# Kernel tuning notes

Measured on AMD Instinct MI355X. Metric: run time of the kernel, lower is better.

## Reference

```python
import jax, jax.numpy as jnp
import numpy as np

N_PAPER, N_AUTHOR = 200000, 100000
D_PAPER, D_AUTHOR = 128, 64
H, OUT = 64, 32
E_CITES, E_WRITES = 4000000, 2000000


def _gcn(x, W, b, src, dst, n):
    # GCNConv with default add_self_loops=True, symmetric normalization
    xl = x @ W
    deg = jnp.zeros((n,), xl.dtype).at[dst].add(1.0) + 1.0  # +1 for self loop
    dis = jax.lax.rsqrt(deg)
    norm = dis[src] * dis[dst]
    out = jax.ops.segment_sum(xl[src] * norm[:, None], dst, num_segments=n)
    out = out + xl * (dis * dis)[:, None]  # self-loop term: norm_ii = 1/deg_i
    return out + b


def _sage(x_src, x_dst, Wl, bl, Wr, src, dst, n_dst):
    # SAGEConv: mean neighbor aggregation -> lin_l, plus root lin_r on dst
    ones = jnp.ones(src.shape, x_src.dtype)
    cnt = jnp.maximum(jax.ops.segment_sum(ones, dst, num_segments=n_dst), 1.0)
    mean = jax.ops.segment_sum(x_src[src], dst, num_segments=n_dst) / cnt[:, None]
    return mean @ Wl + bl + x_dst @ Wr


def _gat(x_src, x_dst, Ws, Wd, a_s, a_d, b, src, dst, n_dst):
    # GATConv heads=1, bipartite, add_self_loops=False, leaky_relu slope 0.2
    xs = x_src @ Ws  # [Ns, H]
    xd = x_dst @ Wd  # [Nd, H]
    a_src = xs @ a_s  # [Ns]
    a_dst = xd @ a_d  # [Nd]
    e = a_src[src] + a_dst[dst]
    e = jnp.where(e > 0, e, 0.2 * e)
    m = jax.ops.segment_max(e, dst, num_segments=n_dst)
    m = jnp.where(jnp.isfinite(m), m, 0.0)  # nodes with no in-edges
    ex = jnp.exp(e - m[dst])
    denom = jax.ops.segment_sum(ex, dst, num_segments=n_dst)
    alpha = ex / denom[dst]
    out = jax.ops.segment_sum(alpha[:, None] * xs[src], dst, num_segments=n_dst)
    return out + b


def _forward(x_paper, x_author, params, cites_src, cites_dst, writes_src, writes_dst):
    for (gW, gb, sWl, sbl, sWr, aWs, aWd, aas, aad, ab) in params:
        p_gcn = _gcn(x_paper, gW, gb, cites_src, cites_dst, N_PAPER)
        p_sage = _sage(x_author, x_paper, sWl, sbl, sWr, writes_src, writes_dst, N_PAPER)
        # rev_writes: paper -> author, i.e. src=writes_dst (paper), dst=writes_src (author)
        a_gat = _gat(x_paper, x_author, aWs, aWd, aas, aad, ab, writes_dst, writes_src, N_AUTHOR)
        x_paper = jax.nn.relu(p_gcn + p_sage)  # HeteroConv aggr='sum'
        x_author = jax.nn.relu(a_gat)
    return x_paper, x_author


def setup_inputs() -> dict:
    key = jax.random.key(0)
    ks = jax.random.split(key, 40)
    rn = lambda i, shp, s=0.1: jax.random.normal(ks[i], shp, jnp.float32) * s
    inp = {}
    inp['x_paper'] = rn(0, (N_PAPER, D_PAPER), 1.0)
    inp['x_author'] = rn(1, (N_AUTHOR, D_AUTHOR), 1.0)
    dims = [(D_PAPER, D_AUTHOR), (H, H)]
    i = 2
    for l, (dp, da) in enumerate(dims):
        inp[f'gcn_W{l}'] = rn(i, (dp, H)); i += 1
        inp[f'gcn_b{l}'] = jnp.zeros((H,), jnp.float32)
        inp[f'sage_Wl{l}'] = rn(i, (da, H)); i += 1
        inp[f'sage_bl{l}'] = jnp.zeros((H,), jnp.float32)
        inp[f'sage_Wr{l}'] = rn(i, (dp, H)); i += 1
        inp[f'gat_Ws{l}'] = rn(i, (dp, H)); i += 1
        inp[f'gat_Wd{l}'] = rn(i, (da, H)); i += 1
        inp[f'gat_as{l}'] = rn(i, (H,)); i += 1
        inp[f'gat_ad{l}'] = rn(i, (H,)); i += 1
        inp[f'gat_b{l}'] = jnp.zeros((H,), jnp.float32)
    inp['lin_W'] = rn(i, (H, OUT)); i += 1
    inp['lin_b'] = jnp.zeros((OUT,), jnp.float32)
    inp['cites_src'] = jax.random.randint(ks[30], (E_CITES,), 0, N_PAPER)
    inp['cites_dst'] = jax.random.randint(ks[31], (E_CITES,), 0, N_PAPER)
    inp['writes_src'] = jax.random.randint(ks[32], (E_WRITES,), 0, N_AUTHOR)
    inp['writes_dst'] = jax.random.randint(ks[33], (E_WRITES,), 0, N_PAPER)
    return inp


def reference(x_paper, x_author,
              gcn_W0, gcn_b0, sage_Wl0, sage_bl0, sage_Wr0,
              gat_Ws0, gat_Wd0, gat_as0, gat_ad0, gat_b0,
              gcn_W1, gcn_b1, sage_Wl1, sage_bl1, sage_Wr1,
              gat_Ws1, gat_Wd1, gat_as1, gat_ad1, gat_b1,
              lin_W, lin_b,
              cites_src, cites_dst, writes_src, writes_dst):
    params = [
        (gcn_W0, gcn_b0, sage_Wl0, sage_bl0, sage_Wr0, gat_Ws0, gat_Wd0, gat_as0, gat_ad0, gat_b0),
        (gcn_W1, gcn_b1, sage_Wl1, sage_bl1, sage_Wr1, gat_Ws1, gat_Wd1, gat_as1, gat_ad1, gat_b1),
    ]
    _, x_author_out = _forward(x_paper, x_author, params, cites_src, cites_dst, writes_src, writes_dst)
    return x_author_out @ lin_W + lin_b
```

## Files before the change

kernel.cpp:

```cpp
#include <hip/hip_runtime.h>
#include <hip/hip_bf16.h>

#define NP 200000
#define NA 100000
#define DP 128
#define HD 64
#define EC 4000000
#define EW 2000000
#define NSCAN (2 * NP + NA)
#define NBUCK 4
#define CAPC 64
#define CAPW 48
#define CAPA 64

typedef __hip_bfloat16 bf16;
typedef __attribute__((ext_vector_type(8))) short short8;
typedef __attribute__((ext_vector_type(4))) float f32x4;

__device__ __forceinline__ float bf2f(bf16 h) { return __bfloat162float(h); }

__device__ __forceinline__ short8 pack8(float4 a, float4 b) {
    union {
        short8 s;
        unsigned u[4];
    } r;
    __hip_bfloat162 h;
    h = __float22bfloat162_rn(float2{a.x, a.y});
    r.u[0] = *reinterpret_cast<unsigned*>(&h);
    h = __float22bfloat162_rn(float2{a.z, a.w});
    r.u[1] = *reinterpret_cast<unsigned*>(&h);
    h = __float22bfloat162_rn(float2{b.x, b.y});
    r.u[2] = *reinterpret_cast<unsigned*>(&h);
    h = __float22bfloat162_rn(float2{b.z, b.w});
    r.u[3] = *reinterpret_cast<unsigned*>(&h);
    return r.s;
}


__global__ __launch_bounds__(256) void fill_pass_kernel(const int* __restrict__ cs,
                                                        const int* __restrict__ cd,
                                                        const int* __restrict__ ws,
                                                        const int* __restrict__ wd,
                                                        int* __restrict__ CUR,
                                                        int* __restrict__ colC,
                                                        int* __restrict__ colWd,
                                                        int* __restrict__ colWa, int bucket) {
    long i = (long)blockIdx.x * 256 + threadIdx.x;
    if (i < EC) {
        int d = __builtin_nontemporal_load(&cd[i]);
        if ((int)(((long)d * NBUCK) / NP) != bucket) return;
        int s = __builtin_nontemporal_load(&cs[i]);
        int pos = atomicAdd(&CUR[d * 4], 1);
        if (pos < CAPC) colC[(size_t)d * CAPC + pos] = s;
    } else if (i < (long)EC + EW) {
        long e = i - EC;
        int d = __builtin_nontemporal_load(&wd[e]);
        int a = __builtin_nontemporal_load(&ws[e]);
        if ((int)(((long)d * NBUCK) / NP) == bucket) {
            int pos = atomicAdd(&CUR[(NP + d) * 4], 1);
            if (pos < CAPW) colWd[(size_t)d * CAPW + pos] = a;
        }
        if ((int)(((long)a * NBUCK) / NA) == bucket) {
            int pos = atomicAdd(&CUR[(2 * NP + a) * 4], 1);
            if (pos < CAPA) colWa[(size_t)a * CAPA + pos] = d;
        }
    }
}


__global__ __launch_bounds__(256) void conv_author_kernel(const float* __restrict__ XA,
                                                          const float* __restrict__ wvec,
                                                          bf16* __restrict__ XAbf,
                                                          float* __restrict__ adst) {
    __shared__ float vs[64];
    if (threadIdx.x < 64) vs[threadIdx.x] = wvec[threadIdx.x];
    __syncthreads();
    int r = blockIdx.x * 4 + (threadIdx.x >> 6);
    int lane = threadIdx.x & 63;
    float x = XA[(size_t)r * 64 + lane];
    XAbf[(size_t)r * 64 + lane] = __float2bfloat16(x);
    float p = x * vs[lane];
#pragma unroll
    for (int o = 32; o > 0; o >>= 1) p += __shfl_xor(p, o, 64);
    if (lane == 0) adst[r] = p;
}


__global__ void wprep_kernel(const float* __restrict__ Wg, const float* __restrict__ Wl,
                             const float* __restrict__ Wr, const float* __restrict__ Ws0,
                             const float* __restrict__ Ws1, short* __restrict__ WF,
                             const float* __restrict__ Wd0, const float* __restrict__ ad0,
                             const float* __restrict__ Wd1, const float* __restrict__ ad1,
                             float* __restrict__ wvec0, float* __restrict__ wvec1) {
    int bid = blockIdx.x;
    int lane = threadIdx.x;
    if (bid >= 64) {
        const float* Wd = (bid == 64) ? Wd0 : Wd1;
        const float* ad = (bid == 64) ? ad0 : ad1;
        float* wv = (bid == 64) ? wvec0 : wvec1;
        float s = 0.f;
        for (int c = 0; c < 64; c++) s += Wd[lane * 64 + c] * ad[c];
        wv[lane] = s;
        return;
    }
    int q = lane & 15, g = lane >> 4;
    int m, r;
    size_t dst;
    if (bid < 16) {
        m = 0; r = bid; dst = 0;
    } else if (bid < 40) {
        m = 1; r = bid - 16; dst = 8192;
    } else if (bid < 56) {
        m = 2; r = bid - 40; dst = 20480;
    } else {
        m = 3; r = bid - 56; dst = 28672;
    }
    int ks = r >> 2, n = r & 3;
    int col = n * 16 + q;
    float v[8];
#pragma unroll
    for (int j = 0; j < 8; j++) {
        int kr = ks * 32 + g * 8 + j;
        float x;
        if (m == 0) x = Wg[(size_t)kr * 64 + col];
        else if (m == 1) x = (kr < 64) ? Wl[(size_t)kr * 64 + col] : Wr[(size_t)(kr - 64) * 64 + col];
        else if (m == 2) x = Ws0[(size_t)kr * 64 + col];
        else x = Ws1[(size_t)kr * 64 + col];
        v[j] = x;
    }
    short8 s = pack8(float4{v[0], v[1], v[2], v[3]}, float4{v[4], v[5], v[6], v[7]});
    *reinterpret_cast<short8*>(WF + dst + ((size_t)r * 64 + lane) * 8) = s;
}


template <int K, int ASTRIDE, bool ABF16, bool ADOT, bool SCALE>
__global__ __launch_bounds__(256) void mfma_gemm_kernel(const void* __restrict__ Xv,
                                                        const short* __restrict__ Wf,
                                                        bf16* __restrict__ outb,
                                                        const float* __restrict__ avec,
                                                        float* __restrict__ adot,
                                                        const int* __restrict__ CURs) {
    int tid = threadIdx.x;
    int lane = tid & 63, q = lane & 15, g = lane >> 4;
    int rw = blockIdx.x * 64 + (tid >> 6) * 16;
    int arow = rw + q;
    f32x4 acc[4];
#pragma unroll
    for (int n = 0; n < 4; n++) acc[n] = f32x4{0.f, 0.f, 0.f, 0.f};
#pragma unroll
    for (int ks = 0; ks < K / 32; ks++) {
        short8 af;
        if constexpr (ABF16) {
            af = *reinterpret_cast<const short8*>((const bf16*)Xv + (size_t)arow * ASTRIDE +
                                                  ks * 32 + g * 8);
        } else {
            const float* xr = (const float*)Xv + (size_t)arow * ASTRIDE + ks * 32 + g * 8;
            float4 a0 = *reinterpret_cast<const float4*>(xr);
            float4 a1 = *reinterpret_cast<const float4*>(xr + 4);
            af = pack8(a0, a1);
        }
#pragma unroll
        for (int n = 0; n < 4; n++) {
            short8 bfr =
                *reinterpret_cast<const short8*>(Wf + ((size_t)(ks * 4 + n) * 64 + lane) * 8);
            acc[n] = __builtin_amdgcn_mfma_f32_16x16x32_bf16(af, bfr, acc[n], 0, 0, 0);
        }
    }
    float av[4];
    if constexpr (ADOT) {
#pragma unroll
        for (int n = 0; n < 4; n++) av[n] = avec[n * 16 + q];
    }
#pragma unroll
    for (int j = 0; j < 4; j++) {
        int R = rw + g * 4 + j;
        float sc = 1.f;
        if constexpr (SCALE) sc = rsqrtf((float)CURs[(unsigned)R * 4] + 1.0f);
#pragma unroll
        for (int n = 0; n < 4; n++) {
            outb[(size_t)R * 64 + n * 16 + q] = __float2bfloat16(acc[n][j] * sc);
        }
        if constexpr (ADOT) {
            float t = acc[0][j] * av[0] + acc[1][j] * av[1] + acc[2][j] * av[2] + acc[3][j] * av[3];
            t += __shfl_xor(t, 1, 64);
            t += __shfl_xor(t, 2, 64);
            t += __shfl_xor(t, 4, 64);
            t += __shfl_xor(t, 8, 64);
            if (q == 0) adot[R] = t;
        }
    }
}


__global__ __launch_bounds__(256) void mfma_sage_kernel(const bf16* B3s,
                                                        const float* __restrict__ XP,
                                                        const float* __restrict__ B2,
                                                        const float* __restrict__ bl,
                                                        const short* __restrict__ Wf, bf16* P1) {
    int tid = threadIdx.x;
    int lane = tid & 63, q = lane & 15, g = lane >> 4;
    int rw = blockIdx.x * 64 + (tid >> 6) * 16;
    int arow = rw + q;
    f32x4 acc[4];
#pragma unroll
    for (int n = 0; n < 4; n++) acc[n] = f32x4{0.f, 0.f, 0.f, 0.f};
#pragma unroll
    for (int ks = 0; ks < 6; ks++) {
        short8 af;
        if (ks < 2) {
            af = *reinterpret_cast<const short8*>(B3s + (size_t)arow * 128 + 64 + ks * 32 + g * 8);
        } else {
            const float* xr = XP + (size_t)arow * DP + (ks - 2) * 32 + g * 8;
            float4 a0 = *reinterpret_cast<const float4*>(xr);
            float4 a1 = *reinterpret_cast<const float4*>(xr + 4);
            af = pack8(a0, a1);
        }
#pragma unroll
        for (int n = 0; n < 4; n++) {
            short8 bfr =
                *reinterpret_cast<const short8*>(Wf + ((size_t)(ks * 4 + n) * 64 + lane) * 8);
            acc[n] = __builtin_amdgcn_mfma_f32_16x16x32_bf16(af, bfr, acc[n], 0, 0, 0);
        }
    }
    float blv[4];
#pragma unroll
    for (int n = 0; n < 4; n++) blv[n] = bl[n * 16 + q];
#pragma unroll
    for (int j = 0; j < 4; j++) {
        int R = rw + g * 4 + j;
#pragma unroll
        for (int n = 0; n < 4; n++) {
            int col = n * 16 + q;
            float v = acc[n][j] + B2[(size_t)R * 64 + col] + blv[n];
            P1[(size_t)R * 128 + col] = __float2bfloat16(fmaxf(v, 0.f));
        }
    }
}


__global__ __launch_bounds__(256) void paper_gather_kernel(const bf16* __restrict__ B1,
                                                           const bf16* __restrict__ XA,
                                                           const int* __restrict__ CUR,
                                                           const int* colC,
                                                           const int* __restrict__ colWd,
                                                           const float* __restrict__ gb,
                                                           float* __restrict__ B2, bf16* B3s) {
    int node = __builtin_amdgcn_readfirstlane(blockIdx.x * 4 + (threadIdx.x >> 6));
    unsigned lane = threadIdx.x & 63;
    int degc_t = CUR[(unsigned)node * 4];
    float dd = rsqrtf((float)degc_t + 1.0f);
    int degc = min(degc_t, CAPC);
    unsigned cb = (unsigned)node * CAPC;
    float acc = bf2f(B1[((unsigned)node << 6) + lane]);
    int e = 0;
    for (; e + 8 <= degc; e += 8) {
        unsigned off[8];
#pragma unroll
        for (int j = 0; j < 8; j++) off[j] = ((unsigned)colC[cb + e + j] << 6) + lane;
        float v[8];
#pragma unroll
        for (int j = 0; j < 8; j++) v[j] = bf2f(B1[off[j]]);
#pragma unroll
        for (int j = 0; j < 8; j++) acc += v[j];
    }
    for (; e + 4 <= degc; e += 4) {
        unsigned o0 = ((unsigned)colC[cb + e] << 6) + lane;
        unsigned o1 = ((unsigned)colC[cb + e + 1] << 6) + lane;
        unsigned o2 = ((unsigned)colC[cb + e + 2] << 6) + lane;
        unsigned o3 = ((unsigned)colC[cb + e + 3] << 6) + lane;
        float v0 = bf2f(B1[o0]), v1 = bf2f(B1[o1]);
        float v2 = bf2f(B1[o2]), v3 = bf2f(B1[o3]);
        acc += v0 + v1;
        acc += v2 + v3;
    }
    for (; e < degc; e++) acc += bf2f(B1[((unsigned)colC[cb + e] << 6) + lane]);
    B2[((unsigned)node << 6) + lane] = acc * dd + gb[lane];
    int degw_t = CUR[((unsigned)NP + node) * 4];
    float ic = 1.0f / fmaxf((float)degw_t, 1.0f);
    int degw = min(degw_t, CAPW);
    unsigned wb = (unsigned)node * CAPW;
    float s = 0.f;
    e = 0;
    for (; e + 8 <= degw; e += 8) {
        unsigned off[8];
#pragma unroll
        for (int j = 0; j < 8; j++) off[j] = ((unsigned)colWd[wb + e + j] << 6) + lane;
        float v[8];
#pragma unroll
        for (int j = 0; j < 8; j++) v[j] = bf2f(XA[off[j]]);
#pragma unroll
        for (int j = 0; j < 8; j++) s += v[j];
    }
    for (; e + 4 <= degw; e += 4) {
        unsigned o0 = ((unsigned)colWd[wb + e] << 6) + lane;
        unsigned o1 = ((unsigned)colWd[wb + e + 1] << 6) + lane;
        unsigned o2 = ((unsigned)colWd[wb + e + 2] << 6) + lane;
        unsigned o3 = ((unsigned)colWd[wb + e + 3] << 6) + lane;
        float v0 = bf2f(XA[o0]), v1 = bf2f(XA[o1]);
        float v2 = bf2f(XA[o2]), v3 = bf2f(XA[o3]);
        s += v0 + v1;
        s += v2 + v3;
    }
    for (; e < degw; e++) s += bf2f(XA[((unsigned)colWd[wb + e] << 6) + lane]);
    B3s[(unsigned)node * 128u + 64u + lane] = __float2bfloat16(s * ic);
}


__device__ __forceinline__ float lrelu(float v) { return v > 0.f ? v : 0.2f * v; }

__device__ __forceinline__ float rl_f(float v, int l) {
    return __int_as_float(__builtin_amdgcn_readlane(__float_as_int(v), l));
}

__device__ __forceinline__ void gat_phase(const bf16* __restrict__ XS, int pi, float xi, int deg,
                                          unsigned lane, float& accO, float& denO) {
    float den = xi;
#pragma unroll
    for (int o = 32; o > 0; o >>= 1) den += __shfl_xor(den, o, 64);
    float acc = 0.f;
    int l = 0;
    for (; l + 8 <= deg; l += 8) {
        float v[8];
#pragma unroll
        for (int j = 0; j < 8; j++) {
            unsigned pl = (unsigned)__builtin_amdgcn_readlane(pi, l + j);
            v[j] = bf2f(XS[(pl << 6) + lane]);
        }
#pragma unroll
        for (int j = 0; j < 8; j++) acc += rl_f(xi, l + j) * v[j];
    }
    for (; l < deg; l++) {
        unsigned pl = (unsigned)__builtin_amdgcn_readlane(pi, l);
        acc += rl_f(xi, l) * bf2f(XS[(pl << 6) + lane]);
    }
    accO = acc;
    denO = den;
}

__global__ __launch_bounds__(256) void gat_fused_kernel(
    const bf16* __restrict__ XS0, const bf16* __restrict__ XS1, const int* __restrict__ CUR,
    const int* __restrict__ colA, const float* __restrict__ asrc0,
    const float* __restrict__ asrc1, const float* __restrict__ adst0,
    const float* __restrict__ ab0, const float* __restrict__ wvec1,
    const float* __restrict__ ab1, const float* __restrict__ linW,
    const float* __restrict__ linb, float* __restrict__ out) {
    __shared__ float Ws[64 * 32];
    __shared__ float vbuf[4][64];
    __shared__ float lbs[32];
    int tid = threadIdx.x;
    for (int i = tid; i < 64 * 32; i += 256) Ws[i] = linW[i];
    if (tid < 32) lbs[tid] = linb[tid];
    __syncthreads();
    int wid = tid >> 6;
    int a = __builtin_amdgcn_readfirstlane(blockIdx.x * 4 + wid);
    unsigned lane = tid & 63;
    int deg = min(CUR[(2u * NP + a) * 4], CAPA);
    unsigned cb = (unsigned)a * CAPA;
    int pi = (lane < (unsigned)deg) ? colA[cb + lane] : 0;
    bool act = lane < (unsigned)deg;
    float x0 = act ? __expf(lrelu(asrc0[(unsigned)pi] + adst0[(unsigned)a])) : 0.f;
    float acc0, den0;
    gat_phase(XS0, pi, x0, deg, lane, acc0, den0);
    float inv0 = den0 > 0.f ? 1.f / den0 : 0.f;
    float val0 = fmaxf(acc0 * inv0 + ab0[lane], 0.f);
    float ada1 = val0 * wvec1[lane];
#pragma unroll
    for (int o = 32; o > 0; o >>= 1) ada1 += __shfl_xor(ada1, o, 64);
    float x1 = act ? __expf(lrelu(asrc1[(unsigned)pi] + ada1)) : 0.f;
    float acc1, den1;
    gat_phase(XS1, pi, x1, deg, lane, acc1, den1);
    float inv1 = den1 > 0.f ? 1.f / den1 : 0.f;
    vbuf[wid][lane] = fmaxf(acc1 * inv1 + ab1[lane], 0.f);
    __syncthreads();
    if (tid < 128) {
        int w = tid >> 5, c = tid & 31;
        int node = blockIdx.x * 4 + w;
        float s = lbs[c];
#pragma unroll
        for (int k = 0; k < 64; k++) s += vbuf[w][k] * Ws[k * 32 + c];
        out[(size_t)node * 32 + c] = s;
    }
}


static inline int cdivi(long a, long b) { return (int)((a + b - 1) / b); }

extern "C" void kernel_launch(void* const* d_in, const int* in_sizes, int n_in, void* d_out,
                              int out_size, void* d_ws, size_t ws_size, hipStream_t stream) {
    const float* x_paper = (const float*)d_in[0];
    const float* x_author = (const float*)d_in[1];
    const float* gcn_W0 = (const float*)d_in[2];
    const float* gcn_b0 = (const float*)d_in[3];
    const float* sage_Wl0 = (const float*)d_in[4];
    const float* sage_bl0 = (const float*)d_in[5];
    const float* sage_Wr0 = (const float*)d_in[6];
    const float* gat_Ws0 = (const float*)d_in[7];
    const float* gat_Wd0 = (const float*)d_in[8];
    const float* gat_as0 = (const float*)d_in[9];
    const float* gat_ad0 = (const float*)d_in[10];
    const float* gat_b0 = (const float*)d_in[11];
    const float* gat_Ws1 = (const float*)d_in[17];
    const float* gat_Wd1 = (const float*)d_in[18];
    const float* gat_as1 = (const float*)d_in[19];
    const float* gat_ad1 = (const float*)d_in[20];
    const float* gat_b1 = (const float*)d_in[21];
    const float* lin_W = (const float*)d_in[22];
    const float* lin_b = (const float*)d_in[23];
    const int* cites_src = (const int*)d_in[24];
    const int* cites_dst = (const int*)d_in[25];
    const int* writes_src = (const int*)d_in[26];
    const int* writes_dst = (const int*)d_in[27];

    float* out = (float*)d_out;

    char* base = (char*)d_ws;
    bf16* BF = (bf16*)base;
    base += (size_t)NP * 64 * 2;
    float* B2 = (float*)base;
    base += (size_t)NP * 64 * 4;
    int* colC = (int*)base;
    bf16* R3 = (bf16*)base;
    base += (size_t)NP * CAPC * 4;
    int* colWd = (int*)base;
    bf16* XS1 = (bf16*)base;
    base += (size_t)NP * CAPW * 4;
    int* colWa = (int*)base;
    base += (size_t)NA * CAPA * 4;
    bf16* XAbf = (bf16*)base;
    base += (size_t)NA * 64 * 2;
    int* CUR = (int*)base;
    base += (size_t)NSCAN * 4 * 4;
    float* asrc0 = (float*)base;
    float* asrc1 = asrc0 + NP;
    float* adst0 = asrc1 + NP;
    float* wvec0 = adst0 + NA;
    float* wvec1 = wvec0 + 64;
    short* WF = (short*)(wvec1 + 64);

    dim3 blk(256);
    const long EMERGED = (long)EC + EW;

    hipMemsetAsync(CUR, 0, (size_t)NSCAN * 4 * 4, stream);
    wprep_kernel<<<66, 64, 0, stream>>>(gcn_W0, sage_Wl0, sage_Wr0, gat_Ws0, gat_Ws1, WF, gat_Wd0,
                                        gat_ad0, gat_Wd1, gat_ad1, wvec0, wvec1);

    for (int b = 0; b < NBUCK; b++) {
        fill_pass_kernel<<<cdivi(EMERGED, 256), blk, 0, stream>>>(cites_src, cites_dst,
                                                                  writes_src, writes_dst, CUR,
                                                                  colC, colWd, colWa, b);
    }

    conv_author_kernel<<<NA / 4, blk, 0, stream>>>(x_author, wvec0, XAbf, adst0);

    mfma_gemm_kernel<DP, DP, false, false, true><<<NP / 64, blk, 0, stream>>>(x_paper, WF, BF,
                                                                              nullptr, nullptr,
                                                                              CUR);
    paper_gather_kernel<<<NP / 4, blk, 0, stream>>>(BF, XAbf, CUR, colC, colWd, gcn_b0, B2, R3);

    mfma_sage_kernel<<<NP / 64, blk, 0, stream>>>(R3, x_paper, B2, sage_bl0, WF + 8192, R3);

    mfma_gemm_kernel<DP, DP, false, true, false><<<NP / 64, blk, 0, stream>>>(
        x_paper, WF + 20480, BF, gat_as0, asrc0, nullptr);
    mfma_gemm_kernel<HD, 128, true, true, false><<<NP / 64, blk, 0, stream>>>(
        R3, WF + 28672, XS1, gat_as1, asrc1, nullptr);

    gat_fused_kernel<<<NA / 4, blk, 0, stream>>>(BF, XS1, CUR, colWa, asrc0, asrc1, adst0, gat_b0,
                                                 wvec1, gat_b1, lin_W, lin_b, out);
}
```

Measured before the change: 794.8 us.

## Fuse GCN and GAT-source GEMMs over x_paper; stage GAT edge weights in LDS

Merges the two separate 128-wide GEMMs on x_paper (the GCN projection and the GAT source projection) into one kernel, so x_paper is read once and both outputs come from the same A fragments. The GAT source features now go to a separate XS0 buffer instead of reusing BF. The GAT aggregation loop now stores (index, weight) pairs in shared memory and reads them back, replacing the per-edge readlane broadcasts, and the denominator reduction moves out of gat_phase. This costs an extra NP*64 bf16 workspace and one more LDS round trip per edge.

```diff
diff --git a/kernel.cpp b/kernel.cpp
--- a/kernel.cpp
+++ b/kernel.cpp
@@ -133,6 +133,63 @@
 }
 
 
+__global__ __launch_bounds__(256) void fused2_gemm_kernel(const float* __restrict__ XP,
+                                                          const short* __restrict__ WFg,
+                                                          const short* __restrict__ WFs,
+                                                          bf16* __restrict__ BF,
+                                                          bf16* __restrict__ XS0,
+                                                          const float* __restrict__ avec,
+                                                          float* __restrict__ adot,
+                                                          const int* __restrict__ CURs) {
+    int tid = threadIdx.x;
+    int lane = tid & 63, q = lane & 15, g = lane >> 4;
+    int rw = blockIdx.x * 64 + (tid >> 6) * 16;
+    int arow = rw + q;
+    f32x4 accg[4], accs[4];
+#pragma unroll
+    for (int n = 0; n < 4; n++) {
+        accg[n] = f32x4{0.f, 0.f, 0.f, 0.f};
+        accs[n] = f32x4{0.f, 0.f, 0.f, 0.f};
+    }
+#pragma unroll
+    for (int ks = 0; ks < 4; ks++) {
+        const float* xr = XP + (size_t)arow * DP + ks * 32 + g * 8;
+        float4 a0 = *reinterpret_cast<const float4*>(xr);
+        float4 a1 = *reinterpret_cast<const float4*>(xr + 4);
+        short8 af = pack8(a0, a1);
+#pragma unroll
+        for (int n = 0; n < 4; n++) {
+            short8 bg = *reinterpret_cast<const short8*>(WFg + ((size_t)(ks * 4 + n) * 64 + lane) * 8);
+            accg[n] = __builtin_amdgcn_mfma_f32_16x16x32_bf16(af, bg, accg[n], 0, 0, 0);
+        }
+#pragma unroll
+        for (int n = 0; n < 4; n++) {
+            short8 bs = *reinterpret_cast<const short8*>(WFs + ((size_t)(ks * 4 + n) * 64 + lane) * 8);
+            accs[n] = __builtin_amdgcn_mfma_f32_16x16x32_bf16(af, bs, accs[n], 0, 0, 0);
+        }
+    }
+    float av[4];
+#pragma unroll
+    for (int n = 0; n < 4; n++) av[n] = avec[n * 16 + q];
+#pragma unroll
+    for (int j = 0; j < 4; j++) {
+        int R = rw + g * 4 + j;
+        float sc = rsqrtf((float)CURs[(unsigned)R * 4] + 1.0f);
+#pragma unroll
+        for (int n = 0; n < 4; n++) {
+            BF[(size_t)R * 64 + n * 16 + q] = __float2bfloat16(accg[n][j] * sc);
+            XS0[(size_t)R * 64 + n * 16 + q] = __float2bfloat16(accs[n][j]);
+        }
+        float t = accs[0][j] * av[0] + accs[1][j] * av[1] + accs[2][j] * av[2] + accs[3][j] * av[3];
+        t += __shfl_xor(t, 1, 64);
+        t += __shfl_xor(t, 2, 64);
+        t += __shfl_xor(t, 4, 64);
+        t += __shfl_xor(t, 8, 64);
+        if (q == 0) adot[R] = t;
+    }
+}
+
+
 template <int K, int ASTRIDE, bool ABF16, bool ADOT, bool SCALE>
 __global__ __launch_bounds__(256) void mfma_gemm_kernel(const void* __restrict__ Xv,
                                                         const short* __restrict__ Wf,
@@ -308,33 +365,26 @@
 
 __device__ __forceinline__ float lrelu(float v) { return v > 0.f ? v : 0.2f * v; }
 
-__device__ __forceinline__ float rl_f(float v, int l) {
-    return __int_as_float(__builtin_amdgcn_readlane(__float_as_int(v), l));
-}
-
-__device__ __forceinline__ void gat_phase(const bf16* __restrict__ XS, int pi, float xi, int deg,
-                                          unsigned lane, float& accO, float& denO) {
-    float den = xi;
-#pragma unroll
-    for (int o = 32; o > 0; o >>= 1) den += __shfl_xor(den, o, 64);
+__device__ __forceinline__ void gat_phase(const bf16* __restrict__ XS, const int2* pxl, int deg,
+                                          unsigned lane, float& accO) {
     float acc = 0.f;
     int l = 0;
     for (; l + 8 <= deg; l += 8) {
-        float v[8];
+        float v[8], x[8];
 #pragma unroll
         for (int j = 0; j < 8; j++) {
-            unsigned pl = (unsigned)__builtin_amdgcn_readlane(pi, l + j);
-            v[j] = bf2f(XS[(pl << 6) + lane]);
-        }
-#pragma unroll
-        for (int j = 0; j < 8; j++) acc += rl_f(xi, l + j) * v[j];
+            int2 px = pxl[l + j];
+            x[j] = __int_as_float(px.y);
+            v[j] = bf2f(XS[((unsigned)px.x << 6) + lane]);
+        }
+#pragma unroll
+        for (int j = 0; j < 8; j++) acc += x[j] * v[j];
     }
     for (; l < deg; l++) {
-        unsigned pl = (unsigned)__builtin_amdgcn_readlane(pi, l);
-        acc += rl_f(xi, l) * bf2f(XS[(pl << 6) + lane]);
+        int2 px = pxl[l];
+        acc += __int_as_float(px.y) * bf2f(XS[((unsigned)px.x << 6) + lane]);
     }
     accO = acc;
-    denO = den;
 }
 
 __global__ __launch_bounds__(256) void gat_fused_kernel(
@@ -347,6 +397,7 @@
     __shared__ float Ws[64 * 32];
     __shared__ float vbuf[4][64];
     __shared__ float lbs[32];
+    __shared__ int2 pxlds[4][64];
     int tid = threadIdx.x;
     for (int i = tid; i < 64 * 32; i += 256) Ws[i] = linW[i];
     if (tid < 32) lbs[tid] = linb[tid];
@@ -359,16 +410,24 @@
     int pi = (lane < (unsigned)deg) ? colA[cb + lane] : 0;
     bool act = lane < (unsigned)deg;
     float x0 = act ? __expf(lrelu(asrc0[(unsigned)pi] + adst0[(unsigned)a])) : 0.f;
-    float acc0, den0;
-    gat_phase(XS0, pi, x0, deg, lane, acc0, den0);
+    float den0 = x0;
+#pragma unroll
+    for (int o = 32; o > 0; o >>= 1) den0 += __shfl_xor(den0, o, 64);
+    pxlds[wid][lane] = int2{pi, __float_as_int(x0)};
+    float acc0;
+    gat_phase(XS0, pxlds[wid], deg, lane, acc0);
     float inv0 = den0 > 0.f ? 1.f / den0 : 0.f;
     float val0 = fmaxf(acc0 * inv0 + ab0[lane], 0.f);
     float ada1 = val0 * wvec1[lane];
 #pragma unroll
     for (int o = 32; o > 0; o >>= 1) ada1 += __shfl_xor(ada1, o, 64);
     float x1 = act ? __expf(lrelu(asrc1[(unsigned)pi] + ada1)) : 0.f;
-    float acc1, den1;
-    gat_phase(XS1, pi, x1, deg, lane, acc1, den1);
+    float den1 = x1;
+#pragma unroll
+    for (int o = 32; o > 0; o >>= 1) den1 += __shfl_xor(den1, o, 64);
+    pxlds[wid][lane] = int2{pi, __float_as_int(x1)};
+    float acc1;
+    gat_phase(XS1, pxlds[wid], deg, lane, acc1);
     float inv1 = den1 > 0.f ? 1.f / den1 : 0.f;
     vbuf[wid][lane] = fmaxf(acc1 * inv1 + ab1[lane], 0.f);
     __syncthreads();
@@ -428,6 +487,8 @@
     base += (size_t)NA * CAPA * 4;
     bf16* XAbf = (bf16*)base;
     base += (size_t)NA * 64 * 2;
+    bf16* XS0 = (bf16*)base;
+    base += (size_t)NP * 64 * 2;
     int* CUR = (int*)base;
     base += (size_t)NSCAN * 4 * 4;
     float* asrc0 = (float*)base;
@@ -452,18 +513,16 @@
 
     conv_author_kernel<<<NA / 4, blk, 0, stream>>>(x_author, wvec0, XAbf, adst0);
 
-    mfma_gemm_kernel<DP, DP, false, false, true><<<NP / 64, blk, 0, stream>>>(x_paper, WF, BF,
-                                                                              nullptr, nullptr,
-                                                                              CUR);
+    fused2_gemm_kernel<<<NP / 64, blk, 0, stream>>>(x_paper, WF, WF + 20480, BF, XS0, gat_as0,
+                                                    asrc0, CUR);
+
     paper_gather_kernel<<<NP / 4, blk, 0, stream>>>(BF, XAbf, CUR, colC, colWd, gcn_b0, B2, R3);
 
     mfma_sage_kernel<<<NP / 64, blk, 0, stream>>>(R3, x_paper, B2, sage_bl0, WF + 8192, R3);
 
-    mfma_gemm_kernel<DP, DP, false, true, false><<<NP / 64, blk, 0, stream>>>(
-        x_paper, WF + 20480, BF, gat_as0, asrc0, nullptr);
     mfma_gemm_kernel<HD, 128, true, true, false><<<NP / 64, blk, 0, stream>>>(
         R3, WF + 28672, XS1, gat_as1, asrc1, nullptr);
 
-    gat_fused_kernel<<<NA / 4, blk, 0, stream>>>(BF, XS1, CUR, colWa, asrc0, asrc1, adst0, gat_b0,
-                                                 wvec1, gat_b1, lin_W, lin_b, out);
-}
+    gat_fused_kernel<<<NA / 4, blk, 0, stream>>>(XS0, XS1, CUR, colWa, asrc0, asrc1, adst0,
+                                                 gat_b0, wvec1, gat_b1, lin_W, lin_b, out);
+}
```

Result: no change. 792.2 us (-0.3%).
